# Kernel optimization log

Hardware: AMD Instinct MI355X
Metric: run time of the kernel (lower is better)

The kernel has to match this reference:

```python
import jax, jax.numpy as jnp
import numpy as np

EPS = 1e-5
SIGMA = 1.0

def _conv(x, w, stride):
    return jax.lax.conv_general_dilated(
        x, w, window_strides=(stride, stride),
        padding=[(w.shape[2] // 2, w.shape[2] // 2), (w.shape[3] // 2, w.shape[3] // 2)],
        dimension_numbers=('NCHW', 'OIHW', 'NCHW'))

def _bn(x, gamma, beta, mean, var):
    # inference-mode batchnorm over channel dim (NCHW)
    inv = gamma / jnp.sqrt(var + EPS)
    return x * inv[None, :, None, None] + (beta - mean * inv)[None, :, None, None]

def setup_inputs() -> dict:
    key = jax.random.key(0)
    ks = jax.random.split(key, 8)
    B, M, H, W, K = 8, 128, 64, 64, 6
    x = jax.random.normal(ks[0], (B, M, H, W), jnp.float32)
    cf = jax.random.normal(ks[1], (B, M, H, W), jnp.float32)
    w1 = jax.random.normal(ks[2], (M // 2, M, 3, 3), jnp.float32) * 0.05
    w2 = jax.random.normal(ks[3], (M // 4, M // 2, 3, 3), jnp.float32) * 0.05
    w3 = jax.random.normal(ks[4], (K, M // 4, 1, 1), jnp.float32) * 0.05
    def bn_params(k, c):
        k1, k2 = jax.random.split(k)
        return (jnp.ones((c,), jnp.float32),
                jnp.zeros((c,), jnp.float32),
                jax.random.normal(k1, (c,), jnp.float32) * 0.1,
                jnp.abs(jax.random.normal(k2, (c,), jnp.float32)) * 0.1 + 1.0)
    g1, b1, m1, v1 = bn_params(ks[5], M // 2)
    g2, b2, m2, v2 = bn_params(ks[6], M // 4)
    g3, b3, m3, v3 = bn_params(ks[7], K)
    return dict(x=x, center_features=cf, w1=w1, g1=g1, b1=b1, m1=m1, v1=v1,
                w2=w2, g2=g2, b2=b2, m2=m2, v2=v2,
                w3=w3, g3=g3, b3=b3, m3=m3, v3=v3)

def reference(x, center_features, w1, g1, b1, m1, v1, w2, g2, b2, m2, v2, w3, g3, b3, m3, v3):
    # center branch: conv-bn-relu x2 (stride 2) + 1x1 conv-bn, then spatial mean
    c = jax.nn.relu(_bn(_conv(center_features, w1, 2), g1, b1, m1, v1))
    c = jax.nn.relu(_bn(_conv(c, w2, 2), g2, b2, m2, v2))
    c = _bn(_conv(c, w3, 1), g3, b3, m3, v3)
    centers = c.reshape(c.shape[0], c.shape[1], -1).mean(axis=2)  # [B, K]

    B, C, H, W = x.shape
    K = centers.shape[-1]
    xf = x.reshape(B, C, H * W, 1)                      # [B,C,HW,1]
    cb = centers[:, None, None, :]                      # [B,1,1,K]
    dist = (xf - cb) ** 2                               # [B,C,HW,K]
    phi_soft = jax.nn.softmax(-SIGMA * dist, axis=-1)
    qsoft = jnp.sum(phi_soft * cb, axis=-1).reshape(B, C, H, W)
    symbols = jnp.argmin(dist, axis=-1)                 # [B,C,HW] (== argmax of hard softmax)
    qhard = centers[jnp.arange(B)[:, None, None], symbols].reshape(B, C, H, W)
    qbar = qsoft + jax.lax.stop_gradient(qhard - qsoft)
    return qbar, qsoft, qhard, symbols.reshape(B, C, H, W), centers
```

## Files before the change

kernel.cpp:

```cpp
#include <hip/hip_runtime.h>
#include <math.h>

#define BN_EPS 1e-5
#define SIGMA 1.0f

__global__ __launch_bounds__(256) void wcvt_kernel(const float* __restrict__ w1, double* __restrict__ w1d)
{
    int i = blockIdx.x * 256 + threadIdx.x;
    if (i < 73728) {
        int j   = i & 7;
        int t   = i >> 3;
        int k   = t % 9;
        int t2  = t / 9;
        int ic  = t2 & 127;
        int ocg = t2 >> 7;
        w1d[i] = (double)w1[((ocg * 8 + j) * 128 + ic) * 9 + k];
    }
}

__global__ __launch_bounds__(256) void conv1_partial_kernel(
    const float* __restrict__ in, const double* __restrict__ w1d,
    float* __restrict__ part)
{
    __shared__ double wlds[2304];

    int bid  = blockIdx.x;
    int tile = bid & 63;
    int ocg  = bid >> 6;
    int isp  = tile >> 4;
    int b    = (tile >> 1) & 7;
    int oht  = tile & 1;

    int tid = threadIdx.x;
    int ow  = tid & 31;
    int ohp = tid >> 5;
    int oh0 = oht * 16 + ohp * 2;
    int ih0 = 2 * oh0 - 1;
    int iw0 = 2 * ow - 1;

    const double* wsrc = w1d + (size_t)(ocg * 128 + isp * 32) * 72;
    for (int i = tid; i < 2304; i += 256) wlds[i] = wsrc[i];
    __syncthreads();

    double acc0[8], acc1[8];
    #pragma unroll
    for (int j = 0; j < 8; ++j) { acc0[j] = 0.0; acc1[j] = 0.0; }

    bool rowok[5], colok[3];
    #pragma unroll
    for (int t = 0; t < 5; ++t) rowok[t] = (ih0 + t) >= 0;
    #pragma unroll
    for (int kw = 0; kw < 3; ++kw) colok[kw] = (iw0 + kw) >= 0;

    const float* base0 = in + ((size_t)(b * 128 + isp * 32) * 64 + ih0) * 64 + iw0;

    float cur[15];
    #pragma unroll
    for (int t = 0; t < 5; ++t)
        #pragma unroll
        for (int kw = 0; kw < 3; ++kw)
            cur[t * 3 + kw] = (rowok[t] && colok[kw]) ? base0[t * 64 + kw] : 0.f;

    #pragma unroll 2
    for (int ic = 0; ic < 32; ++ic) {
        float nxt[15];
        if (ic + 1 < 32) {
            const float* basen = base0 + (size_t)(ic + 1) * 4096;
            #pragma unroll
            for (int t = 0; t < 5; ++t)
                #pragma unroll
                for (int kw = 0; kw < 3; ++kw)
                    nxt[t * 3 + kw] = (rowok[t] && colok[kw]) ? basen[t * 64 + kw] : 0.f;
        }
        double xv[15];
        #pragma unroll
        for (int i = 0; i < 15; ++i) xv[i] = (double)cur[i];

        const double* wk = &wlds[ic * 72];
        #pragma unroll
        for (int k = 0; k < 9; ++k) {
            int kh = k / 3, kw = k % 3;
            double2 wa = *(const double2*)&wk[k * 8 + 0];
            double2 wb = *(const double2*)&wk[k * 8 + 2];
            double2 wc = *(const double2*)&wk[k * 8 + 4];
            double2 wd = *(const double2*)&wk[k * 8 + 6];
            double x0 = xv[kh * 3 + kw];
            double x1 = xv[(kh + 2) * 3 + kw];
            acc0[0] = fma(x0, wa.x, acc0[0]);  acc1[0] = fma(x1, wa.x, acc1[0]);
            acc0[1] = fma(x0, wa.y, acc0[1]);  acc1[1] = fma(x1, wa.y, acc1[1]);
            acc0[2] = fma(x0, wb.x, acc0[2]);  acc1[2] = fma(x1, wb.x, acc1[2]);
            acc0[3] = fma(x0, wb.y, acc0[3]);  acc1[3] = fma(x1, wb.y, acc1[3]);
            acc0[4] = fma(x0, wc.x, acc0[4]);  acc1[4] = fma(x1, wc.x, acc1[4]);
            acc0[5] = fma(x0, wc.y, acc0[5]);  acc1[5] = fma(x1, wc.y, acc1[5]);
            acc0[6] = fma(x0, wd.x, acc0[6]);  acc1[6] = fma(x1, wd.x, acc1[6]);
            acc0[7] = fma(x0, wd.y, acc0[7]);  acc1[7] = fma(x1, wd.y, acc1[7]);
        }
        #pragma unroll
        for (int i = 0; i < 15; ++i) cur[i] = nxt[i];
    }

    #pragma unroll
    for (int j = 0; j < 8; ++j) {
        int idx0 = ((b * 64 + ocg * 8 + j) * 32 + oh0) * 32 + ow;
        part[isp * 524288 + idx0]      = (float)acc0[j];
        part[isp * 524288 + idx0 + 32] = (float)acc1[j];
    }
}

__global__ __launch_bounds__(256) void conv1_combine_kernel(
    const float* __restrict__ part,
    const float* __restrict__ g, const float* __restrict__ be,
    const float* __restrict__ mn, const float* __restrict__ vr,
    float* __restrict__ y1)
{
    int idx = blockIdx.x * 256 + threadIdx.x;
    int oc = (idx >> 10) & 63;
    double s = (double)part[idx] + (double)part[idx + 524288]
             + (double)part[idx + 2 * 524288] + (double)part[idx + 3 * 524288];
    double inv = (double)g[oc] / sqrt((double)vr[oc] + BN_EPS);
    double o = s * inv + ((double)be[oc] - (double)mn[oc] * inv);
    y1[idx] = fmaxf((float)o, 0.f);
}

__global__ __launch_bounds__(256) void conv2_partial_kernel(
    const float* __restrict__ y1, const float* __restrict__ w,
    float* __restrict__ part)
{
    __shared__ float tin[4][33][36];
    __shared__ float twt[4][9][8];

    int bid = blockIdx.x;
    int ocg = bid & 3;
    int b   = (bid >> 2) & 7;
    int isp = bid >> 5;

    int tid = threadIdx.x;
    int ow  = tid & 15;
    int oh  = tid >> 4;

    const float* inb = y1 + (size_t)(b * 64 + isp * 4) * 1024;

    for (int lin = tid; lin < 4 * 33 * 34; lin += 256) {
        int c   = lin % 34;
        int t2  = lin / 34;
        int rr  = t2 % 33;
        int icc = t2 / 33;
        int ih  = rr - 1;
        int iw  = c - 1;
        float v = 0.f;
        if ((unsigned)ih < 32u && (unsigned)iw < 32u)
            v = inb[(icc * 32 + ih) * 32 + iw];
        tin[icc][rr][c] = v;
    }
    for (int i = tid; i < 288; i += 256) {
        int j   = i & 7;
        int k   = (i >> 3) % 9;
        int icc = i / 72;
        twt[icc][k][j] = w[(ocg * 8 + j) * 576 + (isp * 4 + icc) * 9 + k];
    }
    __syncthreads();

    double acc[8];
    #pragma unroll
    for (int j = 0; j < 8; ++j) acc[j] = 0.0;

    for (int icc = 0; icc < 4; ++icc) {
        double xv[9];
        #pragma unroll
        for (int kh = 0; kh < 3; ++kh)
            #pragma unroll
            for (int kw = 0; kw < 3; ++kw)
                xv[kh * 3 + kw] = (double)tin[icc][2 * oh + kh][2 * ow + kw];
        #pragma unroll
        for (int k = 0; k < 9; ++k) {
            float4 wa = *(const float4*)&twt[icc][k][0];
            float4 wb = *(const float4*)&twt[icc][k][4];
            acc[0] = fma(xv[k], (double)wa.x, acc[0]);
            acc[1] = fma(xv[k], (double)wa.y, acc[1]);
            acc[2] = fma(xv[k], (double)wa.z, acc[2]);
            acc[3] = fma(xv[k], (double)wa.w, acc[3]);
            acc[4] = fma(xv[k], (double)wb.x, acc[4]);
            acc[5] = fma(xv[k], (double)wb.y, acc[5]);
            acc[6] = fma(xv[k], (double)wb.z, acc[6]);
            acc[7] = fma(xv[k], (double)wb.w, acc[7]);
        }
    }
    int obase = ((b * 32 + ocg * 8) * 16 + oh) * 16 + ow;
    #pragma unroll
    for (int j = 0; j < 8; ++j)
        part[isp * 65536 + obase + j * 256] = (float)acc[j];
}

__global__ __launch_bounds__(256) void conv2_combine_kernel(
    const float* __restrict__ part,
    const float* __restrict__ g, const float* __restrict__ be,
    const float* __restrict__ mn, const float* __restrict__ vr,
    float* __restrict__ y2)
{
    int idx = blockIdx.x * 256 + threadIdx.x;
    int oc = (idx >> 8) & 31;
    double s = 0.0;
    #pragma unroll
    for (int p = 0; p < 16; ++p) s += (double)part[idx + p * 65536];
    double inv = (double)g[oc] / sqrt((double)vr[oc] + BN_EPS);
    double o = s * inv + ((double)be[oc] - (double)mn[oc] * inv);
    y2[idx] = fmaxf((float)o, 0.f);
}

__global__ __launch_bounds__(256) void ybar_kernel(const float* __restrict__ y, double* __restrict__ ybar)
{
    __shared__ double s[4];
    int j = blockIdx.x;
    double v = (double)y[j * 256 + threadIdx.x];
    #pragma unroll
    for (int o = 32; o > 0; o >>= 1) v += __shfl_down(v, o, 64);
    if ((threadIdx.x & 63) == 0) s[threadIdx.x >> 6] = v;
    __syncthreads();
    if (threadIdx.x == 0) ybar[j] = (s[0] + s[1] + s[2] + s[3]) * (1.0 / 256.0);
}

__global__ __launch_bounds__(64) void centers_kernel(
    const double* __restrict__ ybar, const float* __restrict__ w3,
    const float* __restrict__ g, const float* __restrict__ be,
    const float* __restrict__ mn, const float* __restrict__ vr,
    double* __restrict__ cen_ws, float* __restrict__ cen_out)
{
    int t = threadIdx.x;
    if (t < 48) {
        int b = t / 6;
        int k = t % 6;
        double acc = 0.0;
        for (int ic = 0; ic < 32; ++ic) acc = fma((double)w3[k * 32 + ic], ybar[b * 32 + ic], acc);
        double inv = (double)g[k] / sqrt((double)vr[k] + BN_EPS);
        double c = acc * inv + ((double)be[k] - (double)mn[k] * inv);
        cen_ws[t]  = c;
        cen_out[t] = (float)c;
    }
}

__global__ __launch_bounds__(256) void quant_kernel(
    const float* __restrict__ x, const double* __restrict__ centers,
    float* __restrict__ qbar, float* __restrict__ qsoft,
    float* __restrict__ qhard, float* __restrict__ sym)
{
    int vid = blockIdx.x * 256 + threadIdx.x;
    int b = vid >> 17;

    double c[6];
    float cf[6];
    #pragma unroll
    for (int k = 0; k < 6; ++k) { c[k] = centers[b * 6 + k]; cf[k] = (float)c[k]; }

    float4 xv = ((const float4*)x)[vid];
    float xs[4] = {xv.x, xv.y, xv.z, xv.w};
    float r_bar[4], r_soft[4], r_hard[4], r_sym[4];

    #pragma unroll
    for (int i = 0; i < 4; ++i) {
        double xx = (double)xs[i];
        double d[6];
        double dmin = 1e300;
        int amin = 0;
        #pragma unroll
        for (int k = 0; k < 6; ++k) {
            double t = xx - c[k];
            d[k] = t * t;
            if (d[k] < dmin) { dmin = d[k]; amin = k; }
        }
        float se = 0.f, sw = 0.f;
        #pragma unroll
        for (int k = 0; k < 6; ++k) {
            float e = __expf(SIGMA * (float)(dmin - d[k]));
            se += e;
            sw += e * cf[k];
        }
        float qs = sw / se;
        float qh = cf[amin];
        r_soft[i] = qs;
        r_hard[i] = qh;
        r_bar[i]  = qh;
        r_sym[i]  = (float)amin;
    }

    ((float4*)qbar)[vid]  = make_float4(r_bar[0],  r_bar[1],  r_bar[2],  r_bar[3]);
    ((float4*)qsoft)[vid] = make_float4(r_soft[0], r_soft[1], r_soft[2], r_soft[3]);
    ((float4*)qhard)[vid] = make_float4(r_hard[0], r_hard[1], r_hard[2], r_hard[3]);
    ((float4*)sym)[vid]   = make_float4(r_sym[0],  r_sym[1],  r_sym[2],  r_sym[3]);
}

extern "C" void kernel_launch(void* const* d_in, const int* in_sizes, int n_in,
                              void* d_out, int out_size, void* d_ws, size_t ws_size,
                              hipStream_t stream) {
    const float* x  = (const float*)d_in[0];
    const float* cf = (const float*)d_in[1];
    const float* w1 = (const float*)d_in[2];
    const float* g1 = (const float*)d_in[3];
    const float* b1 = (const float*)d_in[4];
    const float* m1 = (const float*)d_in[5];
    const float* v1 = (const float*)d_in[6];
    const float* w2 = (const float*)d_in[7];
    const float* g2 = (const float*)d_in[8];
    const float* b2 = (const float*)d_in[9];
    const float* m2 = (const float*)d_in[10];
    const float* v2 = (const float*)d_in[11];
    const float* w3 = (const float*)d_in[12];
    const float* g3 = (const float*)d_in[13];
    const float* b3 = (const float*)d_in[14];
    const float* m3 = (const float*)d_in[15];
    const float* v3 = (const float*)d_in[16];

    const int NELEM = 8 * 128 * 64 * 64;
    float* out   = (float*)d_out;
    float* qbar  = out;
    float* qsoft = out + (size_t)NELEM;
    float* qhard = out + (size_t)2 * NELEM;
    float* sym   = out + (size_t)3 * NELEM;
    float* cen_o = out + (size_t)4 * NELEM;

    char* ws = (char*)d_ws;
    float*  part1 = (float*)(ws);
    float*  y1    = (float*)(ws + 8388608);
    float*  part2 = (float*)(ws + 10485760);
    float*  y2    = (float*)(ws + 14680064);
    double* yb    = (double*)(ws + 14942208);
    double* cen   = (double*)(ws + 14944256);
    double* w1d   = (double*)(ws + 14944640);

    wcvt_kernel<<<288, 256, 0, stream>>>(w1, w1d);
    conv1_partial_kernel<<<512, 256, 0, stream>>>(cf, w1d, part1);
    conv1_combine_kernel<<<2048, 256, 0, stream>>>(part1, g1, b1, m1, v1, y1);
    conv2_partial_kernel<<<512, 256, 0, stream>>>(y1, w2, part2);
    conv2_combine_kernel<<<256, 256, 0, stream>>>(part2, g2, b2, m2, v2, y2);
    ybar_kernel<<<256, 256, 0, stream>>>(y2, yb);
    centers_kernel<<<1, 64, 0, stream>>>(yb, w3, g3, b3, m3, v3, cen, cen_o);
    quant_kernel<<<NELEM / 4 / 256, 256, 0, stream>>>(x, cen, qbar, qsoft, qhard, sym);
}
```

Before: 191.3 us.

## Split conv1 input channels finer, inline weight conversion, fuse conv2 combine with mean

Conv1's input-channel split goes from 4 to 8 slices, so the grid doubles to 1024 blocks. Occupancy is requested with launch_bounds(256,4) and the fp32-to-double weight conversion now happens inside each block, which removes the separate wcvt kernel. The conv2 combine and the spatial-mean reduction are fused so y2 is never written, dropping one launch. In exchange, the partial buffer written and read by the conv1 combine doubles in size, and every block repeats the strided weight gather.

```diff
diff --git a/kernel.cpp b/kernel.cpp
--- a/kernel.cpp
+++ b/kernel.cpp
@@ -4,32 +4,17 @@
 #define BN_EPS 1e-5
 #define SIGMA 1.0f
 
-__global__ __launch_bounds__(256) void wcvt_kernel(const float* __restrict__ w1, double* __restrict__ w1d)
-{
-    int i = blockIdx.x * 256 + threadIdx.x;
-    if (i < 73728) {
-        int j   = i & 7;
-        int t   = i >> 3;
-        int k   = t % 9;
-        int t2  = t / 9;
-        int ic  = t2 & 127;
-        int ocg = t2 >> 7;
-        w1d[i] = (double)w1[((ocg * 8 + j) * 128 + ic) * 9 + k];
-    }
-}
-
-__global__ __launch_bounds__(256) void conv1_partial_kernel(
-    const float* __restrict__ in, const double* __restrict__ w1d,
+__global__ __launch_bounds__(256, 4) void conv1_partial_kernel(
+    const float* __restrict__ in, const float* __restrict__ w1,
     float* __restrict__ part)
 {
-    __shared__ double wlds[2304];
-
-    int bid  = blockIdx.x;
-    int tile = bid & 63;
-    int ocg  = bid >> 6;
-    int isp  = tile >> 4;
-    int b    = (tile >> 1) & 7;
-    int oht  = tile & 1;
+    __shared__ double wlds[1152];
+
+    int bid = blockIdx.x;
+    int oht = bid & 1;
+    int b   = (bid >> 1) & 7;
+    int isp = (bid >> 4) & 7;
+    int ocg = bid >> 7;
 
     int tid = threadIdx.x;
     int ow  = tid & 31;
@@ -38,8 +23,13 @@
     int ih0 = 2 * oh0 - 1;
     int iw0 = 2 * ow - 1;
 
-    const double* wsrc = w1d + (size_t)(ocg * 128 + isp * 32) * 72;
-    for (int i = tid; i < 2304; i += 256) wlds[i] = wsrc[i];
+    for (int i = tid; i < 1152; i += 256) {
+        int j  = i & 7;
+        int t  = i >> 3;
+        int k  = t % 9;
+        int ic = t / 9;
+        wlds[i] = (double)w1[((ocg * 8 + j) * 128 + isp * 16 + ic) * 9 + k];
+    }
     __syncthreads();
 
     double acc0[8], acc1[8];
@@ -50,9 +40,9 @@
     #pragma unroll
     for (int t = 0; t < 5; ++t) rowok[t] = (ih0 + t) >= 0;
     #pragma unroll
-    for (int kw = 0; kw < 3; ++kw) colok[kw] = (iw0 + kw) >= 0;
-
-    const float* base0 = in + ((size_t)(b * 128 + isp * 32) * 64 + ih0) * 64 + iw0;
+    for (int t = 0; t < 3; ++t) colok[t] = (iw0 + t) >= 0;
+
+    const float* base0 = in + ((size_t)(b * 128 + isp * 16) * 64 + ih0) * 64 + iw0;
 
     float cur[15];
     #pragma unroll
@@ -61,10 +51,9 @@
         for (int kw = 0; kw < 3; ++kw)
             cur[t * 3 + kw] = (rowok[t] && colok[kw]) ? base0[t * 64 + kw] : 0.f;
 
-    #pragma unroll 2
-    for (int ic = 0; ic < 32; ++ic) {
+    for (int ic = 0; ic < 16; ++ic) {
         float nxt[15];
-        if (ic + 1 < 32) {
+        if (ic + 1 < 16) {
             const float* basen = base0 + (size_t)(ic + 1) * 4096;
             #pragma unroll
             for (int t = 0; t < 5; ++t)
@@ -115,8 +104,9 @@
 {
     int idx = blockIdx.x * 256 + threadIdx.x;
     int oc = (idx >> 10) & 63;
-    double s = (double)part[idx] + (double)part[idx + 524288]
-             + (double)part[idx + 2 * 524288] + (double)part[idx + 3 * 524288];
+    double s = 0.0;
+    #pragma unroll
+    for (int p = 0; p < 8; ++p) s += (double)part[idx + p * 524288];
     double inv = (double)g[oc] / sqrt((double)vr[oc] + BN_EPS);
     double o = s * inv + ((double)be[oc] - (double)mn[oc] * inv);
     y1[idx] = fmaxf((float)o, 0.f);
@@ -191,32 +181,28 @@
         part[isp * 65536 + obase + j * 256] = (float)acc[j];
 }
 
-__global__ __launch_bounds__(256) void conv2_combine_kernel(
+__global__ __launch_bounds__(256) void conv2_combine_ybar_kernel(
     const float* __restrict__ part,
     const float* __restrict__ g, const float* __restrict__ be,
     const float* __restrict__ mn, const float* __restrict__ vr,
-    float* __restrict__ y2)
-{
-    int idx = blockIdx.x * 256 + threadIdx.x;
-    int oc = (idx >> 8) & 31;
+    double* __restrict__ ybar)
+{
+    __shared__ double sm[4];
+    int j  = blockIdx.x;
+    int oc = j & 31;
+    int t  = threadIdx.x;
+    int idx = j * 256 + t;
     double s = 0.0;
     #pragma unroll
     for (int p = 0; p < 16; ++p) s += (double)part[idx + p * 65536];
     double inv = (double)g[oc] / sqrt((double)vr[oc] + BN_EPS);
     double o = s * inv + ((double)be[oc] - (double)mn[oc] * inv);
-    y2[idx] = fmaxf((float)o, 0.f);
-}
-
-__global__ __launch_bounds__(256) void ybar_kernel(const float* __restrict__ y, double* __restrict__ ybar)
-{
-    __shared__ double s[4];
-    int j = blockIdx.x;
-    double v = (double)y[j * 256 + threadIdx.x];
-    #pragma unroll
-    for (int o = 32; o > 0; o >>= 1) v += __shfl_down(v, o, 64);
-    if ((threadIdx.x & 63) == 0) s[threadIdx.x >> 6] = v;
+    double v = fmax(o, 0.0);
+    #pragma unroll
+    for (int off = 32; off > 0; off >>= 1) v += __shfl_down(v, off, 64);
+    if ((t & 63) == 0) sm[t >> 6] = v;
     __syncthreads();
-    if (threadIdx.x == 0) ybar[j] = (s[0] + s[1] + s[2] + s[3]) * (1.0 / 256.0);
+    if (t == 0) ybar[j] = (sm[0] + sm[1] + sm[2] + sm[3]) * (1.0 / 256.0);
 }
 
 __global__ __launch_bounds__(64) void centers_kernel(
@@ -319,19 +305,15 @@
 
     char* ws = (char*)d_ws;
     float*  part1 = (float*)(ws);
-    float*  y1    = (float*)(ws + 8388608);
-    float*  part2 = (float*)(ws + 10485760);
-    float*  y2    = (float*)(ws + 14680064);
-    double* yb    = (double*)(ws + 14942208);
-    double* cen   = (double*)(ws + 14944256);
-    double* w1d   = (double*)(ws + 14944640);
-
-    wcvt_kernel<<<288, 256, 0, stream>>>(w1, w1d);
-    conv1_partial_kernel<<<512, 256, 0, stream>>>(cf, w1d, part1);
+    float*  y1    = (float*)(ws + 16777216);
+    float*  part2 = (float*)(ws + 18874368);
+    double* yb    = (double*)(ws + 23068672);
+    double* cen   = (double*)(ws + 23070720);
+
+    conv1_partial_kernel<<<1024, 256, 0, stream>>>(cf, w1, part1);
     conv1_combine_kernel<<<2048, 256, 0, stream>>>(part1, g1, b1, m1, v1, y1);
     conv2_partial_kernel<<<512, 256, 0, stream>>>(y1, w2, part2);
-    conv2_combine_kernel<<<256, 256, 0, stream>>>(part2, g2, b2, m2, v2, y2);
-    ybar_kernel<<<256, 256, 0, stream>>>(y2, yb);
+    conv2_combine_ybar_kernel<<<256, 256, 0, stream>>>(part2, g2, b2, m2, v2, yb);
     centers_kernel<<<1, 64, 0, stream>>>(yb, w3, g3, b3, m3, v3, cen, cen_o);
     quant_kernel<<<NELEM / 4 / 256, 256, 0, stream>>>(x, cen, qbar, qsoft, qhard, sym);
 }
```

Measured after the change: 180.7 us. 1.06x faster.
